# Kernel tuning notes

Measured on AMD Instinct MI355X. Metric: run time of the kernel, lower is better.

The kernel has to match this reference:

```python
import jax, jax.numpy as jnp
import numpy as np
import math

NUM_EXPERTS = 64
CAPACITY_FACTOR = 1.0


def reference(x, wg):
    # x: [S, D] tokens, wg: [E, D] router weight (torch Linear layout)
    S, D = x.shape
    E = wg.shape[0]
    capacity = int(CAPACITY_FACTOR * math.ceil(S / E))  # training-mode capacity

    logits = jnp.einsum('sd,ed->se', x, wg)              # [S, E]
    gates = jax.nn.softmax(logits, axis=1)               # [S, E]

    indices1_s = jnp.argmax(gates, axis=1)               # [S]
    mask1 = jax.nn.one_hot(indices1_s, E, dtype=gates.dtype)  # [S, E]

    gates1_s = jnp.sum(gates * mask1, axis=1)            # [S]
    locations1 = jnp.cumsum(mask1, axis=0) - 1.0         # fused_cumsum_sub_one, [S, E]

    # load-balancing auxiliary loss
    me = jnp.mean(gates, axis=0)                         # [E]
    ce = jnp.mean(mask1, axis=0)                         # [E]
    l_aux = jnp.mean(me * ce) * (E * E)

    # drop tokens over capacity
    mask1 = mask1 * (locations1 < capacity).astype(mask1.dtype)
    locations1_s = jnp.sum(locations1 * mask1, axis=1).astype(jnp.int32)  # [S]

    gates1 = gates1_s[:, None] * mask1                   # [S, E]
    locations1_sc = jax.nn.one_hot(locations1_s, capacity, dtype=gates1.dtype)  # [S, C]
    # bmm(gates1[:, :, 1], locations1_sc[:, 1, :]) -> outer product per token
    combine1_sec = gates1[:, :, None] * locations1_sc[:, None, :]  # [S, E, C]
    dispatch_mask = combine1_sec.astype(bool)
    return (l_aux, combine1_sec, dispatch_mask)


def setup_inputs() -> dict:
    key = jax.random.key(0)
    k1, k2 = jax.random.split(key)
    x = jax.random.normal(k1, (8192, 2048), dtype=jnp.float32)
    wg = jax.random.normal(k2, (NUM_EXPERTS, 2048), dtype=jnp.float32) * 0.02
    return {"x": x, "wg": wg}
```

## Files before the change

kernel.cpp:

```cpp
#include <hip/hip_runtime.h>
#include <cstdint>
#include <cstddef>

#define S_TOK 8192
#define DIM   2048
#define NE    64
#define CAP   128
#define KSPLIT 2
#define BS    32
#define DT    32

#define OFF_PART   0
#define OFF_IDX    1048576
#define OFF_GATE   1056768
#define OFF_LOC    1064960
#define OFF_MEPART 1073152
#define OFF_PROD   1089536

__global__ __launch_bounds__(256) void gemm_logits(
    const float* __restrict__ x, const float* __restrict__ wg,
    float* __restrict__ part)
{
    __shared__ float xs[BS][DT + 1];
    __shared__ float wsh[NE][DT + 1];

    const int sb  = blockIdx.x * BS;
    const int k   = blockIdx.y;
    const int d0  = k * (DIM / KSPLIT);
    const int tid = threadIdx.x;

    const int s_loc = (tid >> 4) * 2;
    const int e_loc = (tid & 15) * 4;

    float acc[2][4] = {{0.f,0.f,0.f,0.f},{0.f,0.f,0.f,0.f}};

    for (int t = 0; t < DIM / KSPLIT; t += DT) {
        {
            const int r = tid >> 3;
            const int c = (tid & 7) * 4;
            const float4 v = *reinterpret_cast<const float4*>(
                &x[(size_t)(sb + r) * DIM + d0 + t + c]);
            xs[r][c]   = v.x; xs[r][c+1] = v.y;
            xs[r][c+2] = v.z; xs[r][c+3] = v.w;
        }
        {
            const int r = tid >> 2;
            const int c = (tid & 3) * 8;
            const float4 v0 = *reinterpret_cast<const float4*>(
                &wg[(size_t)r * DIM + d0 + t + c]);
            const float4 v1 = *reinterpret_cast<const float4*>(
                &wg[(size_t)r * DIM + d0 + t + c + 4]);
            wsh[r][c]   = v0.x; wsh[r][c+1] = v0.y;
            wsh[r][c+2] = v0.z; wsh[r][c+3] = v0.w;
            wsh[r][c+4] = v1.x; wsh[r][c+5] = v1.y;
            wsh[r][c+6] = v1.z; wsh[r][c+7] = v1.w;
        }
        __syncthreads();
        #pragma unroll
        for (int d = 0; d < DT; ++d) {
            const float xv0 = xs[s_loc][d];
            const float xv1 = xs[s_loc + 1][d];
            const float w0 = wsh[e_loc][d];
            const float w1 = wsh[e_loc + 1][d];
            const float w2 = wsh[e_loc + 2][d];
            const float w3 = wsh[e_loc + 3][d];
            acc[0][0] += xv0 * w0; acc[0][1] += xv0 * w1;
            acc[0][2] += xv0 * w2; acc[0][3] += xv0 * w3;
            acc[1][0] += xv1 * w0; acc[1][1] += xv1 * w1;
            acc[1][2] += xv1 * w2; acc[1][3] += xv1 * w3;
        }
        __syncthreads();
    }
    #pragma unroll
    for (int i = 0; i < 2; ++i)
        #pragma unroll
        for (int j = 0; j < 4; ++j)
            part[((size_t)k * S_TOK + sb + s_loc + i) * NE + e_loc + j] = acc[i][j];
}

__global__ __launch_bounds__(256) void softmax_top1(
    const float* __restrict__ part, int* __restrict__ idx,
    float* __restrict__ gate, float* __restrict__ me_part)
{
    const int lane = threadIdx.x & 63;
    const int wid  = threadIdx.x >> 6;
    const int gw   = blockIdx.x * 4 + wid;

    float me_acc = 0.f;
    for (int s = gw; s < S_TOK; s += 256) {
        const float l = part[(size_t)s * NE + lane]
                      + part[((size_t)S_TOK + s) * NE + lane];
        float m = l;
        #pragma unroll
        for (int o = 32; o; o >>= 1) m = fmaxf(m, __shfl_xor(m, o));
        const float ex = __expf(l - m);
        float sum = ex;
        #pragma unroll
        for (int o = 32; o; o >>= 1) sum += __shfl_xor(sum, o);
        float bv = l; int bi = lane;
        #pragma unroll
        for (int o = 32; o; o >>= 1) {
            const float ov = __shfl_xor(bv, o);
            const int   oi = __shfl_xor(bi, o);
            if (ov > bv || (ov == bv && oi < bi)) { bv = ov; bi = oi; }
        }
        const float g = ex / sum;
        me_acc += g;
        if (lane == bi) {
            idx[s]  = bi;
            gate[s] = g;
        }
    }
    me_part[(size_t)gw * NE + lane] = me_acc;
}

__global__ __launch_bounds__(256) void scan_expert(
    const int* __restrict__ idx, const float* __restrict__ me_part,
    int* __restrict__ loc, float* __restrict__ prod)
{
    const int e    = blockIdx.x;
    const int tid  = threadIdx.x;
    const int lane = tid & 63;
    const int wid  = tid >> 6;
    __shared__ int   wsum[4];
    __shared__ float redf[4];

    float mp = me_part[(size_t)tid * NE + e];
    #pragma unroll
    for (int o = 32; o; o >>= 1) mp += __shfl_xor(mp, o);
    if (lane == 0) redf[wid] = mp;

    int running = 0;
    for (int c = 0; c < S_TOK; c += 256) {
        const int s = c + tid;
        const bool match = (idx[s] == e);
        const unsigned long long b = __ballot(match);
        const int before = __popcll(b & ((1ULL << lane) - 1ULL));
        if (lane == 0) wsum[wid] = __popcll(b);
        __syncthreads();
        int woff = 0;
        #pragma unroll
        for (int w = 0; w < 4; ++w) if (w < wid) woff += wsum[w];
        const int tot = wsum[0] + wsum[1] + wsum[2] + wsum[3];
        if (match) {
            const int pos = running + woff + before;
            loc[s] = (pos < CAP) ? pos : -1;
        }
        running += tot;
        __syncthreads();
    }
    if (tid == 0) {
        const float me = (redf[0] + redf[1] + redf[2] + redf[3]) / (float)S_TOK;
        const float ce = (float)running / (float)S_TOK;
        prod[e] = me * ce;
    }
}

__global__ __launch_bounds__(256) void zero_scatter(
    const int* __restrict__ idx, const int* __restrict__ loc,
    const float* __restrict__ gate, const float* __restrict__ prod,
    float* __restrict__ out)
{
    const int s   = blockIdx.x;
    const int tid = threadIdx.x;
    float* cslab = out + 1 + (size_t)s * (NE * CAP);
    float* dslab = cslab + (size_t)S_TOK * NE * CAP;

    const float4 z = {0.f, 0.f, 0.f, 0.f};
    if (tid < 3)        { cslab[tid]  = 0.f; dslab[tid]  = 0.f; }
    else if (tid == 3)  { cslab[8191] = 0.f; dslab[8191] = 0.f; }
    float4* cb = reinterpret_cast<float4*>(cslab + 3);
    float4* db = reinterpret_cast<float4*>(dslab + 3);
    #pragma unroll
    for (int j = tid; j < 2047; j += 256) { cb[j] = z; db[j] = z; }

    __syncthreads();

    if (tid == 0) {
        const int l = loc[s];
        if (l >= 0) {
            const int t = idx[s] * CAP + l;
            cslab[t] = gate[s];
            dslab[t] = 1.0f;
        }
    }
    if (s == 0 && tid >= 64 && tid < 128) {
        const int ln = tid - 64;
        float p = prod[ln];
        #pragma unroll
        for (int o = 32; o; o >>= 1) p += __shfl_xor(p, o);
        if (ln == 0) out[0] = p * (float)NE;
    }
}

extern "C" void kernel_launch(void* const* d_in, const int* in_sizes, int n_in,
                              void* d_out, int out_size, void* d_ws, size_t ws_size,
                              hipStream_t stream)
{
    const float* x  = (const float*)d_in[0];
    const float* wg = (const float*)d_in[1];
    float* out = (float*)d_out;
    float* ws  = (float*)d_ws;

    float* part    = ws + OFF_PART;
    int*   idx     = (int*)(ws + OFF_IDX);
    float* gate    = ws + OFF_GATE;
    int*   loc     = (int*)(ws + OFF_LOC);
    float* me_part = ws + OFF_MEPART;
    float* prod    = ws + OFF_PROD;

    dim3 ggrid(S_TOK / BS, KSPLIT);
    gemm_logits<<<ggrid, 256, 0, stream>>>(x, wg, part);
    softmax_top1<<<64, 256, 0, stream>>>(part, idx, gate, me_part);
    scan_expert<<<NE, 256, 0, stream>>>(idx, me_part, loc, prod);
    zero_scatter<<<S_TOK, 256, 0, stream>>>(idx, loc, gate, prod, out);
}
```

Measured before the change: 693.6 us.

## Retile router GEMM to 64-token blocks with 4x4 register tiles and split-K 4

The logits GEMM now processes 64 tokens per block, with each thread computing a 4x4 output tile. It uses float4 shared-memory reads, stores the weight tile transposed in LDS, and splits K four ways for more blocks. The softmax kernel is launched with twice as many blocks and sums four partials, and the scan kernel combines twice as many me partials. This is meant to raise arithmetic intensity and parallelism in the GEMM, at the cost of more partial-sum traffic and a larger workspace. The dominant cost is likely the large zero_scatter output write, which is unchanged, so the overall effect may be limited.

```diff
diff --git a/kernel.cpp b/kernel.cpp
--- a/kernel.cpp
+++ b/kernel.cpp
@@ -6,76 +6,83 @@
 #define DIM   2048
 #define NE    64
 #define CAP   128
-#define KSPLIT 2
-#define BS    32
+#define KSPLIT 4
+#define BS    64
 #define DT    32
+#define XW    36
+#define WW    68
 
 #define OFF_PART   0
-#define OFF_IDX    1048576
-#define OFF_GATE   1056768
-#define OFF_LOC    1064960
-#define OFF_MEPART 1073152
-#define OFF_PROD   1089536
+#define OFF_IDX    2097152
+#define OFF_GATE   2105344
+#define OFF_LOC    2113536
+#define OFF_MEPART 2121728
+#define OFF_PROD   2154496
 
 __global__ __launch_bounds__(256) void gemm_logits(
     const float* __restrict__ x, const float* __restrict__ wg,
     float* __restrict__ part)
 {
-    __shared__ float xs[BS][DT + 1];
-    __shared__ float wsh[NE][DT + 1];
+    __shared__ float xs[BS][XW];
+    __shared__ float wshT[DT][WW];
 
     const int sb  = blockIdx.x * BS;
     const int k   = blockIdx.y;
     const int d0  = k * (DIM / KSPLIT);
     const int tid = threadIdx.x;
 
-    const int s_loc = (tid >> 4) * 2;
-    const int e_loc = (tid & 15) * 4;
-
-    float acc[2][4] = {{0.f,0.f,0.f,0.f},{0.f,0.f,0.f,0.f}};
+    const int r = tid >> 3;
+    const int c = (tid & 7) * 4;
+    const int ti = tid >> 4;
+    const int ei = tid & 15;
+
+    float4 acc4[4];
+    #pragma unroll
+    for (int i = 0; i < 4; ++i) acc4[i] = make_float4(0.f, 0.f, 0.f, 0.f);
 
     for (int t = 0; t < DIM / KSPLIT; t += DT) {
         {
-            const int r = tid >> 3;
-            const int c = (tid & 7) * 4;
-            const float4 v = *reinterpret_cast<const float4*>(
+            const float4 xa = *reinterpret_cast<const float4*>(
                 &x[(size_t)(sb + r) * DIM + d0 + t + c]);
-            xs[r][c]   = v.x; xs[r][c+1] = v.y;
-            xs[r][c+2] = v.z; xs[r][c+3] = v.w;
+            const float4 xb = *reinterpret_cast<const float4*>(
+                &x[(size_t)(sb + r + 32) * DIM + d0 + t + c]);
+            *reinterpret_cast<float4*>(&xs[r][c])      = xa;
+            *reinterpret_cast<float4*>(&xs[r + 32][c]) = xb;
         }
         {
-            const int r = tid >> 2;
-            const int c = (tid & 3) * 8;
-            const float4 v0 = *reinterpret_cast<const float4*>(
+            const float4 w0 = *reinterpret_cast<const float4*>(
                 &wg[(size_t)r * DIM + d0 + t + c]);
-            const float4 v1 = *reinterpret_cast<const float4*>(
-                &wg[(size_t)r * DIM + d0 + t + c + 4]);
-            wsh[r][c]   = v0.x; wsh[r][c+1] = v0.y;
-            wsh[r][c+2] = v0.z; wsh[r][c+3] = v0.w;
-            wsh[r][c+4] = v1.x; wsh[r][c+5] = v1.y;
-            wsh[r][c+6] = v1.z; wsh[r][c+7] = v1.w;
-        }
-        __syncthreads();
-        #pragma unroll
-        for (int d = 0; d < DT; ++d) {
-            const float xv0 = xs[s_loc][d];
-            const float xv1 = xs[s_loc + 1][d];
-            const float w0 = wsh[e_loc][d];
-            const float w1 = wsh[e_loc + 1][d];
-            const float w2 = wsh[e_loc + 2][d];
-            const float w3 = wsh[e_loc + 3][d];
-            acc[0][0] += xv0 * w0; acc[0][1] += xv0 * w1;
-            acc[0][2] += xv0 * w2; acc[0][3] += xv0 * w3;
-            acc[1][0] += xv1 * w0; acc[1][1] += xv1 * w1;
-            acc[1][2] += xv1 * w2; acc[1][3] += xv1 * w3;
-        }
-        __syncthreads();
-    }
-    #pragma unroll
-    for (int i = 0; i < 2; ++i)
-        #pragma unroll
-        for (int j = 0; j < 4; ++j)
-            part[((size_t)k * S_TOK + sb + s_loc + i) * NE + e_loc + j] = acc[i][j];
+            const float4 w1 = *reinterpret_cast<const float4*>(
+                &wg[(size_t)(r + 32) * DIM + d0 + t + c]);
+            wshT[c + 0][r] = w0.x; wshT[c + 1][r] = w0.y;
+            wshT[c + 2][r] = w0.z; wshT[c + 3][r] = w0.w;
+            wshT[c + 0][r + 32] = w1.x; wshT[c + 1][r + 32] = w1.y;
+            wshT[c + 2][r + 32] = w1.z; wshT[c + 3][r + 32] = w1.w;
+        }
+        __syncthreads();
+        #pragma unroll
+        for (int dq = 0; dq < DT / 4; ++dq) {
+            float4 xv[4], wv[4];
+            #pragma unroll
+            for (int i = 0; i < 4; ++i)
+                xv[i] = *reinterpret_cast<const float4*>(&xs[ti * 4 + i][dq * 4]);
+            #pragma unroll
+            for (int q = 0; q < 4; ++q)
+                wv[q] = *reinterpret_cast<const float4*>(&wshT[dq * 4 + q][ei * 4]);
+            #pragma unroll
+            for (int i = 0; i < 4; ++i) {
+                acc4[i].x += xv[i].x*wv[0].x + xv[i].y*wv[1].x + xv[i].z*wv[2].x + xv[i].w*wv[3].x;
+                acc4[i].y += xv[i].x*wv[0].y + xv[i].y*wv[1].y + xv[i].z*wv[2].y + xv[i].w*wv[3].y;
+                acc4[i].z += xv[i].x*wv[0].z + xv[i].y*wv[1].z + xv[i].z*wv[2].z + xv[i].w*wv[3].z;
+                acc4[i].w += xv[i].x*wv[0].w + xv[i].y*wv[1].w + xv[i].z*wv[2].w + xv[i].w*wv[3].w;
+            }
+        }
+        __syncthreads();
+    }
+    #pragma unroll
+    for (int i = 0; i < 4; ++i)
+        *reinterpret_cast<float4*>(
+            &part[((size_t)k * S_TOK + sb + ti * 4 + i) * NE + ei * 4]) = acc4[i];
 }
 
 __global__ __launch_bounds__(256) void softmax_top1(
@@ -87,9 +94,11 @@
     const int gw   = blockIdx.x * 4 + wid;
 
     float me_acc = 0.f;
-    for (int s = gw; s < S_TOK; s += 256) {
-        const float l = part[(size_t)s * NE + lane]
-                      + part[((size_t)S_TOK + s) * NE + lane];
+    for (int s = gw; s < S_TOK; s += 512) {
+        float l = 0.f;
+        #pragma unroll
+        for (int k = 0; k < KSPLIT; ++k)
+            l += part[((size_t)k * S_TOK + s) * NE + lane];
         float m = l;
         #pragma unroll
         for (int o = 32; o; o >>= 1) m = fmaxf(m, __shfl_xor(m, o));
@@ -125,7 +134,7 @@
     __shared__ int   wsum[4];
     __shared__ float redf[4];
 
-    float mp = me_part[(size_t)tid * NE + e];
+    float mp = me_part[(size_t)tid * NE + e] + me_part[(size_t)(tid + 256) * NE + e];
     #pragma unroll
     for (int o = 32; o; o >>= 1) mp += __shfl_xor(mp, o);
     if (lane == 0) redf[wid] = mp;
@@ -211,7 +220,7 @@
 
     dim3 ggrid(S_TOK / BS, KSPLIT);
     gemm_logits<<<ggrid, 256, 0, stream>>>(x, wg, part);
-    softmax_top1<<<64, 256, 0, stream>>>(part, idx, gate, me_part);
+    softmax_top1<<<128, 256, 0, stream>>>(part, idx, gate, me_part);
     scan_expert<<<NE, 256, 0, stream>>>(idx, me_part, loc, prod);
     zero_scatter<<<S_TOK, 256, 0, stream>>>(idx, loc, gate, prod, out);
 }
```

Result: faster. 635.7 us (-8.3%).
